# Optimization experiments

Measured on AMD Instinct MI355X. Metric: run time of the kernel, lower is better.

The kernel has to match this reference:

```python
import jax, jax.numpy as jnp
import numpy as np

# (vocab_size, offset, length) per feature id; alternating single/multi-valued
FEATURE_SPECS = [(100000, 0, 1), (100000, 1, 20), (100000, 21, 1), (100000, 22, 20),
                 (100000, 42, 1), (100000, 43, 20), (100000, 63, 1), (100000, 64, 20),
                 (100000, 84, 1), (100000, 85, 20), (100000, 105, 1), (100000, 106, 20),
                 (100000, 126, 1), (100000, 127, 20), (100000, 147, 1), (100000, 148, 20)]
GROUPS = [[0, 1, 2, 3], [4, 5, 6, 7], [8, 9, 10, 11], [12, 13, 14, 15]]
B, NF, V, E, D, G = 4096, 16, 100001, 64, 512, 4
TOTAL_INT_DIM = 168
LN_EPS = 1e-5


def setup_inputs() -> dict:
    key = jax.random.key(0)
    k0, k1, k2, k3 = jax.random.split(key, 4)
    int_feats = jax.random.randint(k0, (B, TOTAL_INT_DIM), 0, V, dtype=jnp.int32)
    emb_tables = jax.random.normal(k1, (NF, V, E), dtype=jnp.float32) * 0.02
    W = jax.random.normal(k2, (G, len(GROUPS[0]) * E, D), dtype=jnp.float32) * 0.02
    b = jnp.zeros((G, D), dtype=jnp.float32)
    gamma = jnp.ones((G, D), dtype=jnp.float32)
    beta = jnp.zeros((G, D), dtype=jnp.float32)
    return {"int_feats": int_feats, "emb_tables": emb_tables, "W": W, "b": b,
            "gamma": gamma, "beta": beta}


def _forward(int_feats, emb_tables, W, b, gamma, beta):
    # padding_idx=0 -> row 0 is zero (also makes grads to row 0 vanish)
    tables = emb_tables.at[:, 0, :].set(0.0)
    fid_embs = []
    for i, (vs, off, length) in enumerate(FEATURE_SPECS):
        if length == 1:
            e = tables[i][int_feats[:, off]]                       # (B, E)
        else:
            vals = int_feats[:, off:off + length]                  # (B, L)
            emb = tables[i][vals]                                  # (B, L, E)
            mask = (vals != 0).astype(emb.dtype)[..., None]        # (B, L, 1)
            cnt = jnp.clip(mask.sum(axis=1), 1.0)                  # (B, 1)
            e = (emb * mask).sum(axis=1) / cnt                     # (B, E)
        fid_embs.append(e)
    tokens = []
    for g, grp in enumerate(GROUPS):
        cat = jnp.concatenate([fid_embs[j] for j in grp], axis=-1)  # (B, 4*E)
        h = cat @ W[g] + b[g]                                       # (B, D)
        mu = h.mean(axis=-1, keepdims=True)
        var = ((h - mu) ** 2).mean(axis=-1, keepdims=True)          # biased, as torch LN
        hn = (h - mu) / jnp.sqrt(var + LN_EPS) * gamma[g] + beta[g]
        tokens.append(jax.nn.silu(hn))
    return jnp.stack(tokens, axis=1)                                # (B, G, D)


def reference(int_feats, emb_tables, W, b, gamma, beta):
    return _forward(int_feats, emb_tables, W, b, gamma, beta)
```

## Files before the change

### kernel.cpp

```cpp
#include <hip/hip_runtime.h>
#include <hip/hip_bf16.h>

typedef __attribute__((ext_vector_type(8))) short short8;
typedef __attribute__((ext_vector_type(4))) float f32x4;

#define V_TAB 100001
#define B_N   4096

__global__ __launch_bounds__(256) void pool_kernel(
    const int* __restrict__ feats,
    const float* __restrict__ tables,
    __hip_bfloat16* __restrict__ pooled)
{
    const int b    = blockIdx.x;
    const int p    = blockIdx.y * 4 + (threadIdx.x >> 6);
    const int lane = threadIdx.x & 63;
    const int* fr  = feats + b * 168 + p * 21;
    const float* tab_s = tables + (size_t)(2 * p) * (V_TAB * 64);
    const float* tab_m = tab_s + (size_t)(V_TAB * 64);

    const int idx_s = fr[0];
    const float v_s = tab_s[(size_t)idx_s * 64 + lane];

    int   idxs[20];
    float vals[20];
    #pragma unroll
    for (int j = 0; j < 20; ++j) idxs[j] = fr[1 + j];
    #pragma unroll
    for (int j = 0; j < 20; ++j) vals[j] = tab_m[(size_t)idxs[j] * 64 + lane];

    float acc = 0.f; int cnt = 0;
    #pragma unroll
    for (int j = 0; j < 20; ++j)
        if (idxs[j] != 0) { acc += vals[j]; ++cnt; }
    acc *= 1.f / (float)(cnt > 0 ? cnt : 1);

    __hip_bfloat16* orow = pooled + ((size_t)b * 16 + 2 * p) * 64;
    orow[lane]      = __float2bfloat16((idx_s != 0) ? v_s : 0.f);
    orow[64 + lane] = __float2bfloat16(acc);
}

__global__ __launch_bounds__(256) void wprep_kernel(
    const float* __restrict__ W,
    __hip_bfloat16* __restrict__ Wsw)
{
    const int idx = blockIdx.x * 256 + threadIdx.x;
    const int n   = idx & 511;
    const int kk  = (idx >> 9) & 255;
    const int g   = idx >> 17;
    const int w   = n >> 7;
    const int nt  = (n >> 4) & 7;
    const int l15 = n & 15;
    const int ks  = kk >> 5;
    const int lg  = (kk >> 3) & 3;
    const int j   = kk & 7;
    const int lane = lg * 16 + l15;
    const int dst = ((((g * 4 + w) * 8 + nt) * 8 + ks) * 64 + lane) * 8 + j;
    Wsw[dst] = __float2bfloat16(W[idx]);
}

__global__ __launch_bounds__(256, 2) void gemm_ln_silu(
    const __hip_bfloat16* __restrict__ pooled,
    const __hip_bfloat16* __restrict__ Wsw,
    const float* __restrict__ bias,
    const float* __restrict__ gamma,
    const float* __restrict__ beta,
    float* __restrict__ out)
{
    const int g       = blockIdx.y;
    const int rowbase = blockIdx.x * 32;
    const int wave = threadIdx.x >> 6;
    const int lane = threadIdx.x & 63;
    const int l15  = lane & 15;
    const int lg   = lane >> 4;
    const int wcol = wave * 128;

    __shared__ short lds_a[32 * 264];
    {
        const int r  = threadIdx.x >> 3;
        const int c0 = threadIdx.x & 7;
        const short* src = (const short*)pooled + (size_t)(rowbase + r) * 1024 + g * 256;
        #pragma unroll
        for (int i = 0; i < 4; ++i) {
            const int c = c0 + i * 8;
            *(short8*)(lds_a + r * 264 + c * 8) = *(const short8*)(src + c * 8);
        }
    }
    __syncthreads();

    f32x4 acc[2][8];
    #pragma unroll
    for (int mt = 0; mt < 2; ++mt)
        #pragma unroll
        for (int nt = 0; nt < 8; ++nt) acc[mt][nt] = (f32x4){0.f, 0.f, 0.f, 0.f};

    const short* wptr = (const short*)Wsw + ((size_t)(g * 4 + wave) * 4096 + lane) * 8;

    short8 bcur[8], bnxt[8];
    #pragma unroll
    for (int nt = 0; nt < 8; ++nt)
        bcur[nt] = *(const short8*)(wptr + (size_t)(nt * 8) * 512);

    #pragma unroll 1
    for (int ks = 0; ks < 8; ++ks) {
        if (ks < 7) {
            #pragma unroll
            for (int nt = 0; nt < 8; ++nt)
                bnxt[nt] = *(const short8*)(wptr + (size_t)(nt * 8 + ks + 1) * 512);
        }
        const short8 a0 = *(const short8*)(lds_a + l15 * 264 + ks * 32 + lg * 8);
        const short8 a1 = *(const short8*)(lds_a + (16 + l15) * 264 + ks * 32 + lg * 8);
        #pragma unroll
        for (int nt = 0; nt < 8; ++nt) {
            acc[0][nt] = __builtin_amdgcn_mfma_f32_16x16x32_bf16(a0, bcur[nt], acc[0][nt], 0, 0, 0);
            acc[1][nt] = __builtin_amdgcn_mfma_f32_16x16x32_bf16(a1, bcur[nt], acc[1][nt], 0, 0, 0);
        }
        #pragma unroll
        for (int nt = 0; nt < 8; ++nt) bcur[nt] = bnxt[nt];
    }

    float gv[8], tv[8];
    #pragma unroll
    for (int nt = 0; nt < 8; ++nt) {
        const int col = wcol + nt * 16 + l15;
        const float bv = bias[g * 512 + col];
        gv[nt] = gamma[g * 512 + col];
        tv[nt] = beta[g * 512 + col];
        #pragma unroll
        for (int r = 0; r < 4; ++r) { acc[0][nt][r] += bv; acc[1][nt][r] += bv; }
    }

    __shared__ float red[32][4][2];
    #pragma unroll
    for (int mt = 0; mt < 2; ++mt)
        #pragma unroll
        for (int r = 0; r < 4; ++r) {
            float s = 0.f, q = 0.f;
            #pragma unroll
            for (int nt = 0; nt < 8; ++nt) { const float v = acc[mt][nt][r]; s += v; q += v * v; }
            #pragma unroll
            for (int m = 1; m < 16; m <<= 1) { s += __shfl_xor(s, m); q += __shfl_xor(q, m); }
            if (l15 == 0) {
                const int row = mt * 16 + lg * 4 + r;
                red[row][wave][0] = s;
                red[row][wave][1] = q;
            }
        }
    __syncthreads();

    __shared__ float mu_s[32], ri_s[32];
    if (threadIdx.x < 32) {
        const int row = threadIdx.x;
        const float s = red[row][0][0] + red[row][1][0] + red[row][2][0] + red[row][3][0];
        const float q = red[row][0][1] + red[row][1][1] + red[row][2][1] + red[row][3][1];
        const float mu  = s * (1.f / 512.f);
        const float var = q * (1.f / 512.f) - mu * mu;
        mu_s[row] = mu;
        ri_s[row] = rsqrtf(var + 1e-5f);
    }
    __syncthreads();

    #pragma unroll
    for (int mt = 0; mt < 2; ++mt)
        #pragma unroll
        for (int r = 0; r < 4; ++r) {
            const int row = mt * 16 + lg * 4 + r;
            const float mu = mu_s[row];
            const float ri = ri_s[row];
            float* orow = out + ((size_t)(rowbase + row) * 4 + g) * 512 + wcol;
            #pragma unroll
            for (int nt = 0; nt < 8; ++nt) {
                const float h  = acc[mt][nt][r];
                const float hn = (h - mu) * ri * gv[nt] + tv[nt];
                orow[nt * 16 + l15] = hn / (1.f + __expf(-hn));
            }
        }
}

extern "C" void kernel_launch(void* const* d_in, const int* in_sizes, int n_in,
                              void* d_out, int out_size, void* d_ws, size_t ws_size,
                              hipStream_t stream) {
    const int*   feats  = (const int*)d_in[0];
    const float* tables = (const float*)d_in[1];
    const float* W      = (const float*)d_in[2];
    const float* bias   = (const float*)d_in[3];
    const float* gamma  = (const float*)d_in[4];
    const float* beta   = (const float*)d_in[5];
    float* out = (float*)d_out;

    __hip_bfloat16* pooled = (__hip_bfloat16*)d_ws;
    __hip_bfloat16* Wsw    = (__hip_bfloat16*)((char*)d_ws + (size_t)B_N * 16 * 64 * 2);

    pool_kernel<<<dim3(B_N, 2), dim3(256), 0, stream>>>(feats, tables, pooled);
    wprep_kernel<<<dim3(2048), dim3(256), 0, stream>>>(W, Wsw);
    gemm_ln_silu<<<dim3(128, 4), dim3(256), 0, stream>>>(pooled, Wsw, bias, gamma, beta, out);
}
```

Baseline: 505.4 us.

## Fuse embedding gather-pooling into the GEMM+LayerNorm+SiLU kernel

Removes the separate pooling kernel and gathers and mean-pools embeddings directly into LDS inside the GEMM kernel, one group per block. This eliminates the pooled bf16 intermediate write/read and one kernel launch. In exchange, the gather work now runs on only 512 blocks, with each wave processing 8 rows serially, reducing memory-level parallelism for the latency-bound random table reads.

```diff
diff --git a/kernel.cpp b/kernel.cpp
--- a/kernel.cpp
+++ b/kernel.cpp
@@ -6,39 +6,6 @@
 
 #define V_TAB 100001
 #define B_N   4096
-
-__global__ __launch_bounds__(256) void pool_kernel(
-    const int* __restrict__ feats,
-    const float* __restrict__ tables,
-    __hip_bfloat16* __restrict__ pooled)
-{
-    const int b    = blockIdx.x;
-    const int p    = blockIdx.y * 4 + (threadIdx.x >> 6);
-    const int lane = threadIdx.x & 63;
-    const int* fr  = feats + b * 168 + p * 21;
-    const float* tab_s = tables + (size_t)(2 * p) * (V_TAB * 64);
-    const float* tab_m = tab_s + (size_t)(V_TAB * 64);
-
-    const int idx_s = fr[0];
-    const float v_s = tab_s[(size_t)idx_s * 64 + lane];
-
-    int   idxs[20];
-    float vals[20];
-    #pragma unroll
-    for (int j = 0; j < 20; ++j) idxs[j] = fr[1 + j];
-    #pragma unroll
-    for (int j = 0; j < 20; ++j) vals[j] = tab_m[(size_t)idxs[j] * 64 + lane];
-
-    float acc = 0.f; int cnt = 0;
-    #pragma unroll
-    for (int j = 0; j < 20; ++j)
-        if (idxs[j] != 0) { acc += vals[j]; ++cnt; }
-    acc *= 1.f / (float)(cnt > 0 ? cnt : 1);
-
-    __hip_bfloat16* orow = pooled + ((size_t)b * 16 + 2 * p) * 64;
-    orow[lane]      = __float2bfloat16((idx_s != 0) ? v_s : 0.f);
-    orow[64 + lane] = __float2bfloat16(acc);
-}
 
 __global__ __launch_bounds__(256) void wprep_kernel(
     const float* __restrict__ W,
@@ -59,8 +26,9 @@
     Wsw[dst] = __float2bfloat16(W[idx]);
 }
 
-__global__ __launch_bounds__(256, 2) void gemm_ln_silu(
-    const __hip_bfloat16* __restrict__ pooled,
+__global__ __launch_bounds__(256, 2) void fused_pool_gemm_ln(
+    const int* __restrict__ feats,
+    const float* __restrict__ tables,
     const __hip_bfloat16* __restrict__ Wsw,
     const float* __restrict__ bias,
     const float* __restrict__ gamma,
@@ -76,15 +44,47 @@
     const int wcol = wave * 128;
 
     __shared__ short lds_a[32 * 264];
-    {
-        const int r  = threadIdx.x >> 3;
-        const int c0 = threadIdx.x & 7;
-        const short* src = (const short*)pooled + (size_t)(rowbase + r) * 1024 + g * 256;
+
+    const size_t TSZ = (size_t)V_TAB * 64;
+    const float* t0 = tables + (size_t)(4 * g) * TSZ;
+    const float* t1 = t0 + TSZ;
+    const float* t2 = t1 + TSZ;
+    const float* t3 = t2 + TSZ;
+
+    #pragma unroll 1
+    for (int rr = 0; rr < 8; ++rr) {
+        const int r = wave * 8 + rr;
+        const int* fr = feats + (size_t)(rowbase + r) * 168 + g * 42;
+
+        const int i0 = fr[0];
+        const int i2 = fr[21];
+        int idx1[20], idx3[20];
         #pragma unroll
-        for (int i = 0; i < 4; ++i) {
-            const int c = c0 + i * 8;
-            *(short8*)(lds_a + r * 264 + c * 8) = *(const short8*)(src + c * 8);
+        for (int j = 0; j < 20; ++j) { idx1[j] = fr[1 + j]; idx3[j] = fr[22 + j]; }
+
+        const float v0 = t0[(size_t)i0 * 64 + lane];
+        const float v2 = t2[(size_t)i2 * 64 + lane];
+        float v1[20], v3[20];
+        #pragma unroll
+        for (int j = 0; j < 20; ++j) {
+            v1[j] = t1[(size_t)idx1[j] * 64 + lane];
+            v3[j] = t3[(size_t)idx3[j] * 64 + lane];
         }
+
+        float a1 = 0.f, a3 = 0.f; int c1 = 0, c3 = 0;
+        #pragma unroll
+        for (int j = 0; j < 20; ++j) {
+            if (idx1[j] != 0) { a1 += v1[j]; ++c1; }
+            if (idx3[j] != 0) { a3 += v3[j]; ++c3; }
+        }
+        a1 *= 1.f / (float)(c1 > 0 ? c1 : 1);
+        a3 *= 1.f / (float)(c3 > 0 ? c3 : 1);
+
+        short* arow = lds_a + r * 264;
+        ((__hip_bfloat16*)arow)[lane]       = __float2bfloat16(i0 != 0 ? v0 : 0.f);
+        ((__hip_bfloat16*)arow)[64 + lane]  = __float2bfloat16(a1);
+        ((__hip_bfloat16*)arow)[128 + lane] = __float2bfloat16(i2 != 0 ? v2 : 0.f);
+        ((__hip_bfloat16*)arow)[192 + lane] = __float2bfloat16(a3);
     }
     __syncthreads();
 
@@ -188,10 +188,9 @@
     const float* beta   = (const float*)d_in[5];
     float* out = (float*)d_out;
 
-    __hip_bfloat16* pooled = (__hip_bfloat16*)d_ws;
-    __hip_bfloat16* Wsw    = (__hip_bfloat16*)((char*)d_ws + (size_t)B_N * 16 * 64 * 2);
+    __hip_bfloat16* Wsw = (__hip_bfloat16*)d_ws;
 
-    pool_kernel<<<dim3(B_N, 2), dim3(256), 0, stream>>>(feats, tables, pooled);
     wprep_kernel<<<dim3(2048), dim3(256), 0, stream>>>(W, Wsw);
-    gemm_ln_silu<<<dim3(128, 4), dim3(256), 0, stream>>>(pooled, Wsw, bias, gamma, beta, out);
+    fused_pool_gemm_ln<<<dim3(128, 4), dim3(256), 0, stream>>>(
+        feats, tables, Wsw, bias, gamma, beta, out);
 }
```

Measured after the change: 500.0 us. About the same (-1.1%).
